# Optimization experiments

Hardware: AMD Instinct MI355X
Metric: run time of the kernel (lower is better)

## Reference

```python
import jax, jax.numpy as jnp
import numpy as np

B, T, D = 4, 2048, 2048
K, D_B, TOPK, WINDOW = 7, 128, 16, 64
GATE_CAP = 1.0
STRAND_CAP = 1.0
_PHI = 1.618033988749895
_PSI = -0.6180339887498949


def _ln(x, g, b, eps=1e-5):
    m = jnp.mean(x, axis=-1, keepdims=True)
    v = jnp.mean((x - m) ** 2, axis=-1, keepdims=True)
    return (x - m) * jax.lax.rsqrt(v + eps) * g + b


def setup_inputs() -> dict:
    ks = jax.random.split(jax.random.key(0), 20)
    rn = lambda k, s, sc=1.0: jax.random.normal(k, s, jnp.float32) * sc
    d_s = 1.0 / np.sqrt(D)
    db_s = 1.0 / np.sqrt(D_B)
    return {
        'X_write': rn(ks[0], (B, T, D)),
        'X_read': rn(ks[1], (B, T, D)),
        'slots': rn(ks[2], (B, K, D_B)),
        'W0': rn(ks[3], (D, D), d_s),
        'ln_write_g': jnp.ones((D,), jnp.float32),
        'ln_write_b': jnp.zeros((D,), jnp.float32),
        'Wv': rn(ks[4], (D_B, D), d_s),
        'Wk': rn(ks[5], (D_B, D_B), db_s),
        'slot_key_bias': rn(ks[6], (K, D_B), 2.0),
        'Wg_w': rn(ks[7], (D_B, 2 * D_B), 1.0 / np.sqrt(2 * D_B)),
        'Wg_b': jnp.full((D_B,), -2.0, jnp.float32),
        'ln_strand_g': jnp.ones((D_B,), jnp.float32),
        'ln_strand_b': jnp.zeros((D_B,), jnp.float32),
        'Wsq': rn(ks[8], (D_B, D_B), db_s),
        'Wsk': rn(ks[9], (D_B, D_B), db_s),
        'Wsv': rn(ks[10], (D_B, D_B), db_s),
        'lambda_strand': rn(ks[11], (D_B,), 0.1),
        'Wq_read': rn(ks[12], (D_B, D), d_s),
        'Wk_read': rn(ks[13], (D_B, D_B), db_s),
        'Wv_read': rn(ks[14], (D, D_B), db_s),
        'render_coeffs': rn(ks[15], (K, 3, D), 0.1),
        'slot_temps': 1.0 + rn(ks[16], (K,), 0.1),
    }


def reference(X_write, X_read, slots, W0, ln_write_g, ln_write_b, Wv, Wk,
              slot_key_bias, Wg_w, Wg_b, ln_strand_g, ln_strand_b,
              Wsq, Wsk, Wsv, lambda_strand, Wq_read, Wk_read, Wv_read,
              render_coeffs, slot_temps):
    b, t, d = X_write.shape
    sd = 1.0 / np.sqrt(D_B)
    X_n = _ln(X_write, ln_write_g, ln_write_b)

    # --- banded salience + topk (torch.no_grad region; only int indices escape) ---
    W_eff = min(WINDOW, t - 1)
    Xs = jax.lax.stop_gradient(X_n)
    X_W0 = Xs @ jax.lax.stop_gradient(W0).T            # [b,t,d]
    Xp = jnp.pad(X_W0, ((0, 0), (W_eff, 0), (0, 0)))   # left-pad so offset w -> j = i + w - W

    def band_dot(w):
        return jnp.einsum('btd,btd->bt', Xs,
                          jax.lax.dynamic_slice_in_dim(Xp, w, t, axis=1))

    band = jax.vmap(band_dot)(jnp.arange(W_eff)).transpose(1, 2, 0)  # [b,t,W]
    ii = jnp.arange(t)[:, None]
    ww = jnp.arange(W_eff)[None, :]
    jj = ii + ww - W_eff
    valid = (jj >= 0) & (ii >= 1)                      # j in [max(0,i-W), i)
    sal = jnp.where(valid, band, -jnp.inf).reshape(b, -1)
    topk_eff = min(TOPK, t * (t - 1) // 2)
    _, idx = jax.lax.top_k(sal, topk_eff)              # [b,topk]
    i_idx = idx // W_eff
    j_idx = i_idx + (idx % W_eff) - W_eff

    # --- topk pair gather + bilinear relation ---
    x_new = jnp.take_along_axis(X_n, i_idx[..., None], axis=1)  # [b,topk,d]
    x_old = jnp.take_along_axis(X_n, j_idx[..., None], axis=1)
    pair_sal = jnp.sum(x_new * (x_old @ jax.lax.stop_gradient(W0).T), axis=-1)
    alpha = jax.nn.softmax(pair_sal, axis=-1)
    R_t = jnp.einsum('bp,bpe->be', alpha, (x_new - x_old) @ Wv.T)  # [b,d_b]

    # --- slot write ---
    slot_keys = slots @ Wk.T + slot_key_bias[None]
    compat = jnp.einsum('bke,be->bk', slot_keys, R_t) * sd
    compat = compat * jax.nn.softplus(slot_temps)[None]
    sw = jax.nn.softmax(compat, axis=-1)
    weighted_R = sw[..., None] * R_t[:, None, :]                 # [b,K,d_b]
    g = jax.nn.sigmoid(jnp.concatenate([slots, weighted_R], -1) @ Wg_w.T + Wg_b)
    slots_upd = (1.0 - g) * slots + g * weighted_R

    # --- strand mixer (KxK self-attention) ---
    B_ln = _ln(slots_upd, ln_strand_g, ln_strand_b)
    att = jax.nn.softmax(jnp.einsum('bke,bme->bkm', B_ln @ Wsq.T, B_ln @ Wsk.T) * sd, axis=-1)
    ctx = att @ (B_ln @ Wsv.T)
    slots_next = slots_upd + ctx * jnp.clip(jnp.tanh(lambda_strand), -STRAND_CAP, STRAND_CAP)

    # --- aux losses ---
    L_persist = jnp.mean((slots_next - slots) ** 2)
    nrm = jnp.linalg.norm(slots_next, axis=-1, keepdims=True)
    Bn = slots_next / jnp.maximum(nrm, 1e-12)
    cos = jnp.einsum('bke,bme->bkm', Bn, Bn)
    off = 1.0 - jnp.eye(K, dtype=cos.dtype)
    L_div = jnp.sum(cos ** 2 * off) / (b * K * (K - 1))

    # --- directional render gate + read ---
    q_r = X_read @ Wq_read.T                    # [b,t,d_b]
    k_r = slots_next @ Wk_read.T                # [b,K,d_b]
    v_r = slots_next @ Wv_read.T                # [b,K,d]
    scores = jnp.einsum('bte,bke->btk', q_r, k_r) * sd
    q_mean = jnp.mean(X_read, axis=1)           # [b,d]
    w0q = q_mean @ jax.lax.stop_gradient(W0).T
    dphi = _PHI - _PSI
    phi_q = (w0q - _PSI * q_mean) / dphi
    psi_q = (_PHI * q_mean - w0q) / dphi
    pm = jnp.linalg.norm(phi_q, axis=-1, keepdims=True)
    sm = jnp.linalg.norm(psi_q, axis=-1, keepdims=True)
    tot = pm + sm + 1e-6
    basis = jnp.concatenate([jnp.ones_like(pm), pm / tot, sm / tot], axis=-1)  # [b,3]
    gate = jnp.clip(jnp.tanh(jnp.einsum('bi,kid->bkd', basis, render_coeffs)),
                    -GATE_CAP, GATE_CAP)
    z = jnp.einsum('btk,bkd->btd', jax.nn.softmax(scores, axis=-1), v_r * gate)
    return z, slots_next, L_persist, L_div
```

## Files before the change

kernel.cpp:

```cpp
#include <hip/hip_runtime.h>
#include <cstdint>
#include <cstddef>

#define DEV __device__ __forceinline__

typedef __bf16 bf16x8 __attribute__((ext_vector_type(8)));
typedef float f32x4 __attribute__((ext_vector_type(4)));
typedef unsigned short u16;
typedef unsigned int u32;

constexpr int Bq = 4, Tq = 2048, Dq = 2048, Kq = 7, DB = 128, TK = 16;
constexpr float SD = 0.08838834764831845f;
constexpr float PHIc = 1.618033988749895f;
constexpr float PSIc = -0.6180339887498949f;
constexpr float DPHI = 2.2360679774997896f;
#define NEG_INF (-__builtin_inff())

DEV u16 f2bf(float f) {
  union { float f; u32 u; } x; x.f = f;
  u32 r = (x.u + 0x7fffu + ((x.u >> 16) & 1u)) >> 16;
  return (u16)r;
}
DEV float bfbits2f(u32 h) { union { u32 u; float f; } x; x.u = h << 16; return x.f; }

DEV void async16(void* l, const void* g) {
  __builtin_amdgcn_global_load_lds((const __attribute__((address_space(1))) void*)g,
                                   (__attribute__((address_space(3))) void*)l, 16, 0, 0);
}

__global__ __launch_bounds__(256) void k_w0b(const float* __restrict__ W0, u16* __restrict__ W0b) {
  size_t i = ((size_t)blockIdx.x * 256 + threadIdx.x) * 8;
  float4 a = *(const float4*)&W0[i];
  float4 c = *(const float4*)&W0[i + 4];
  u32 p0 = (u32)f2bf(a.x) | ((u32)f2bf(a.y) << 16);
  u32 p1 = (u32)f2bf(a.z) | ((u32)f2bf(a.w) << 16);
  u32 p2 = (u32)f2bf(c.x) | ((u32)f2bf(c.y) << 16);
  u32 p3 = (u32)f2bf(c.z) | ((u32)f2bf(c.w) << 16);
  uint4 st; st.x = p0; st.y = p1; st.z = p2; st.w = p3;
  *(uint4*)&W0b[i] = st;
}

__global__ __launch_bounds__(256) void k_ln(const float* __restrict__ X, const float* __restrict__ g,
                                            const float* __restrict__ bb, u16* __restrict__ Xn) {
  int row = blockIdx.x;
  const float* xr = X + (size_t)row * Dq;
  int tid = threadIdx.x, lane = tid & 63, w = tid >> 6;
  float4 a = *(const float4*)&xr[tid * 8];
  float4 c = *(const float4*)&xr[tid * 8 + 4];
  float s = a.x + a.y + a.z + a.w + c.x + c.y + c.z + c.w;
  float q = a.x*a.x + a.y*a.y + a.z*a.z + a.w*a.w + c.x*c.x + c.y*c.y + c.z*c.z + c.w*c.w;
  #pragma unroll
  for (int o = 32; o; o >>= 1) { s += __shfl_xor(s, o); q += __shfl_xor(q, o); }
  __shared__ float red[8];
  if (lane == 0) { red[w] = s; red[w + 4] = q; }
  __syncthreads();
  float S = red[0] + red[1] + red[2] + red[3];
  float Q = red[4] + red[5] + red[6] + red[7];
  float mean = S * (1.0f / Dq);
  float var = Q * (1.0f / Dq) - mean * mean;
  float rstd = rsqrtf(var + 1e-5f);
  float v[8] = {a.x, a.y, a.z, a.w, c.x, c.y, c.z, c.w};
  u32 p[4];
  #pragma unroll
  for (int j = 0; j < 4; ++j) {
    int d0 = tid * 8 + j * 2;
    float o0 = (v[j*2]   - mean) * rstd * g[d0]   + bb[d0];
    float o1 = (v[j*2+1] - mean) * rstd * g[d0+1] + bb[d0+1];
    p[j] = (u32)f2bf(o0) | ((u32)f2bf(o1) << 16);
  }
  uint4 st; st.x = p[0]; st.y = p[1]; st.z = p[2]; st.w = p[3];
  *(uint4*)&Xn[(size_t)row * Dq + tid * 8] = st;
}

__global__ __launch_bounds__(256) void k_qmean1(const float* __restrict__ X, float* __restrict__ part) {
  int s = blockIdx.x;
  int y = blockIdx.y;
  int b = blockIdx.z;
  int tid = threadIdx.x;
  const float* xb = X + (size_t)b * Tq * Dq + (size_t)s * 1024 + tid * 4;
  f32x4 acc = {0.f, 0.f, 0.f, 0.f};
  #pragma unroll 4
  for (int t = 0; t < 64; ++t) {
    const float4 v = *(const float4*)&xb[(size_t)(y * 64 + t) * Dq];
    acc[0] += v.x; acc[1] += v.y; acc[2] += v.z; acc[3] += v.w;
  }
  float4 st; st.x = acc[0]; st.y = acc[1]; st.z = acc[2]; st.w = acc[3];
  *(float4*)&part[((size_t)(b * 32 + y)) * Dq + s * 1024 + tid * 4] = st;
}

__global__ __launch_bounds__(256) void k_qmean2(const float* __restrict__ part, float* __restrict__ qm) {
  int s = blockIdx.x, b = blockIdx.y, tid = threadIdx.x;
  int col = s * 1024 + tid * 4;
  f32x4 acc = {0.f, 0.f, 0.f, 0.f};
  #pragma unroll 8
  for (int y = 0; y < 32; ++y) {
    float4 v = *(const float4*)&part[((size_t)(b * 32 + y)) * Dq + col];
    acc[0] += v.x; acc[1] += v.y; acc[2] += v.z; acc[3] += v.w;
  }
  float4 st;
  st.x = acc[0] * (1.0f / Tq); st.y = acc[1] * (1.0f / Tq);
  st.z = acc[2] * (1.0f / Tq); st.w = acc[3] * (1.0f / Tq);
  *(float4*)&qm[(size_t)b * Dq + col] = st;
}

__global__ __launch_bounds__(256) void k_w0q(const float* __restrict__ W0, const float* __restrict__ qm,
                                             float* __restrict__ w0q) {
  __shared__ float qs[4][Dq];
  int tid = threadIdx.x, lane = tid & 63, w = tid >> 6;
  for (int i = tid * 4; i < 4 * Dq; i += 1024) {
    *(float4*)&((float*)qs)[i] = *(const float4*)&qm[i];
  }
  __syncthreads();
  #pragma unroll
  for (int r = 0; r < 8; ++r) {
    int d = blockIdx.x * 32 + w * 8 + r;
    const float* wr = W0 + (size_t)d * Dq;
    float a0 = 0, a1 = 0, a2 = 0, a3 = 0;
    for (int e = lane * 4; e < Dq; e += 256) {
      float4 wv = *(const float4*)&wr[e];
      float4 q0 = *(const float4*)&qs[0][e];
      float4 q1 = *(const float4*)&qs[1][e];
      float4 q2 = *(const float4*)&qs[2][e];
      float4 q3 = *(const float4*)&qs[3][e];
      a0 += wv.x*q0.x + wv.y*q0.y + wv.z*q0.z + wv.w*q0.w;
      a1 += wv.x*q1.x + wv.y*q1.y + wv.z*q1.z + wv.w*q1.w;
      a2 += wv.x*q2.x + wv.y*q2.y + wv.z*q2.z + wv.w*q2.w;
      a3 += wv.x*q3.x + wv.y*q3.y + wv.z*q3.z + wv.w*q3.w;
    }
    #pragma unroll
    for (int o = 32; o; o >>= 1) {
      a0 += __shfl_xor(a0, o); a1 += __shfl_xor(a1, o);
      a2 += __shfl_xor(a2, o); a3 += __shfl_xor(a3, o);
    }
    if (lane == 0) {
      w0q[0 * Dq + d] = a0; w0q[1 * Dq + d] = a1;
      w0q[2 * Dq + d] = a2; w0q[3 * Dq + d] = a3;
    }
  }
}

__global__ __launch_bounds__(256) void k_basis(const float* __restrict__ qm, const float* __restrict__ w0q,
                                               float* __restrict__ basis) {
  int tid = threadIdx.x;
  __shared__ float red[256];
  __shared__ float psum;
  for (int b = 0; b < 4; ++b) {
    float ps = 0, ss = 0;
    for (int d = tid; d < Dq; d += 256) {
      float qv = qm[b * Dq + d], wv = w0q[b * Dq + d];
      float ph = (wv - PSIc * qv) * (1.0f / DPHI);
      float pv = (PHIc * qv - wv) * (1.0f / DPHI);
      ps += ph * ph; ss += pv * pv;
    }
    red[tid] = ps; __syncthreads();
    for (int st = 128; st; st >>= 1) { if (tid < st) red[tid] += red[tid + st]; __syncthreads(); }
    if (tid == 0) psum = red[0];
    __syncthreads();
    red[tid] = ss; __syncthreads();
    for (int st = 128; st; st >>= 1) { if (tid < st) red[tid] += red[tid + st]; __syncthreads(); }
    if (tid == 0) {
      float pm = sqrtf(psum), sm = sqrtf(red[0]);
      float tot = pm + sm + 1e-6f;
      basis[b * 3 + 0] = 1.0f; basis[b * 3 + 1] = pm / tot; basis[b * 3 + 2] = sm / tot;
    }
    __syncthreads();
  }
}

__global__ __launch_bounds__(256) void k_gemm(const u16* __restrict__ A, const u16* __restrict__ B,
                                              u16* __restrict__ C, int M, int N, int K) {
  __shared__ u16 As[128 * 64], Bs[128 * 64];
  int tid = threadIdx.x, lane = tid & 63, w = tid >> 6, wr = w >> 1, wc = w & 1;
  int bm = blockIdx.x, bn = blockIdx.y;
  const u16* Ab = A + (size_t)bm * 128 * K;
  const u16* Bb = B + (size_t)bn * 128 * K;
  f32x4 zero = {0.f, 0.f, 0.f, 0.f};
  f32x4 acc[4][4];
  #pragma unroll
  for (int mi = 0; mi < 4; ++mi)
    #pragma unroll
    for (int ni = 0; ni < 4; ++ni) acc[mi][ni] = zero;
  int ro = tid >> 3;
  int co = (tid & 7) * 8;
  int cs = co ^ ((ro & 7) * 8);
  for (int k0 = 0; k0 < K; k0 += 64) {
    #pragma unroll
    for (int i = 0; i < 4; ++i) {
      int row = ro + i * 32;
      async16(&As[row * 64 + co], Ab + (size_t)row * K + k0 + cs);
      async16(&Bs[row * 64 + co], Bb + (size_t)row * K + k0 + cs);
    }
    __syncthreads();
    #pragma unroll
    for (int ks = 0; ks < 2; ++ks) {
      int cbase = ks * 32 + ((lane >> 4) * 8);
      int crd = cbase ^ ((lane & 7) * 8);
      bf16x8 af[4], bfr[4];
      #pragma unroll
      for (int mi = 0; mi < 4; ++mi)
        af[mi] = *(const bf16x8*)&As[(wr * 64 + mi * 16 + (lane & 15)) * 64 + crd];
      #pragma unroll
      for (int ni = 0; ni < 4; ++ni)
        bfr[ni] = *(const bf16x8*)&Bs[(wc * 64 + ni * 16 + (lane & 15)) * 64 + crd];
      #pragma unroll
      for (int mi = 0; mi < 4; ++mi)
        #pragma unroll
        for (int ni = 0; ni < 4; ++ni)
          acc[mi][ni] = __builtin_amdgcn_mfma_f32_16x16x32_bf16(af[mi], bfr[ni], acc[mi][ni], 0, 0, 0);
    }
    __syncthreads();
  }
  int r0 = bm * 128 + wr * 64, c0 = bn * 128 + wc * 64;
  #pragma unroll
  for (int mi = 0; mi < 4; ++mi)
    #pragma unroll
    for (int ni = 0; ni < 4; ++ni) {
      int col = c0 + ni * 16 + (lane & 15);
      int rb = r0 + mi * 16 + ((lane >> 4) * 4);
      #pragma unroll
      for (int rg = 0; rg < 4; ++rg)
        C[(size_t)(rb + rg) * N + col] = f2bf(acc[mi][ni][rg]);
    }
}

__global__ __launch_bounds__(512) void k_band(const u16* __restrict__ Xn, const u16* __restrict__ XW0,
                                              float* __restrict__ sal) {
  int b = blockIdx.y, i0 = blockIdx.x * 32;
  int tid = threadIdx.x, lane = tid & 63, w = tid >> 6;
  int mi0, ni0, mi1 = -1, ni1 = -1;
  if (w < 4)      { mi0 = 0; ni0 = w;     mi1 = 1; ni1 = w + 2; }
  else if (w < 6) { mi0 = 0; ni0 = w; }
  else            { mi0 = 1; ni0 = w - 6; }
  const u16* Xb = Xn + (size_t)b * Tq * Dq;
  const u16* Wb = XW0 + (size_t)b * Tq * Dq;
  int koff = (lane >> 4) * 8;
  const u16* ap0 = Xb + (size_t)(i0 + mi0 * 16 + (lane & 15)) * Dq + koff;
  const u16* ap1 = Xb + (size_t)(i0 + 16 + (lane & 15)) * Dq + koff;
  int j0 = i0 - 64 + ni0 * 16 + (lane & 15); j0 = min(max(j0, 0), Tq - 1);
  int j1 = i0 - 64 + (ni1 < 0 ? 0 : ni1) * 16 + (lane & 15); j1 = min(max(j1, 0), Tq - 1);
  const u16* bp0 = Wb + (size_t)j0 * Dq + koff;
  const u16* bp1 = Wb + (size_t)j1 * Dq + koff;
  f32x4 zero = {0.f, 0.f, 0.f, 0.f};
  f32x4 acc0 = zero, acc1 = zero;
  if (mi1 >= 0) {
    for (int k = 0; k < Dq; k += 32) {
      bf16x8 a0 = *(const bf16x8*)(ap0 + k);
      bf16x8 b0 = *(const bf16x8*)(bp0 + k);
      acc0 = __builtin_amdgcn_mfma_f32_16x16x32_bf16(a0, b0, acc0, 0, 0, 0);
      bf16x8 a1 = *(const bf16x8*)(ap1 + k);
      bf16x8 b1 = *(const bf16x8*)(bp1 + k);
      acc1 = __builtin_amdgcn_mfma_f32_16x16x32_bf16(a1, b1, acc1, 0, 0, 0);
    }
  } else {
    for (int k = 0; k < Dq; k += 32) {
      bf16x8 a0 = *(const bf16x8*)(ap0 + k);
      bf16x8 b0 = *(const bf16x8*)(bp0 + k);
      acc0 = __builtin_amdgcn_mfma_f32_16x16x32_bf16(a0, b0, acc0, 0, 0, 0);
    }
  }
  auto store_tile = [&](int mi, int ni, const f32x4& acc) {
    int nl = ni * 16 + (lane & 15);
    #pragma unroll
    for (int rg = 0; rg < 4; ++rg) {
      int i = i0 + mi * 16 + (lane >> 4) * 4 + rg;
      int wb = nl - (i - i0);
      if (wb >= 0 && wb < 64) {
        int j = i0 - 64 + nl;
        bool valid = (j >= 0) && (i >= 1);
        sal[((size_t)b * Tq + i) * 64 + wb] = valid ? acc[rg] : NEG_INF;
      }
    }
  };
  store_tile(mi0, ni0, acc0);
  if (mi1 >= 0) store_tile(mi1, ni1, acc1);
}

__global__ __launch_bounds__(256) void k_topk1(const float* __restrict__ sal,
                                               float* __restrict__ cv, int* __restrict__ ci) {
  int b = blockIdx.y, chunk = blockIdx.x;
  int tid = threadIdx.x, lane = tid & 63;
  const float* s = sal + (size_t)b * Tq * 64 + (size_t)chunk * 1024;
  float lv[4]; int li[4];
  #pragma unroll
  for (int i = 0; i < 4; ++i) { lv[i] = NEG_INF; li[i] = -1; }
  #pragma unroll
  for (int i = 0; i < 4; ++i) {
    int e = tid + i * 256;
    float v = s[e];
    int idx = chunk * 1024 + e;
    if (v > lv[3]) {
      lv[3] = v; li[3] = idx;
      #pragma unroll
      for (int q = 3; q > 0; --q)
        if (lv[q] > lv[q - 1]) {
          float tv = lv[q]; lv[q] = lv[q - 1]; lv[q - 1] = tv;
          int t2 = li[q]; li[q] = li[q - 1]; li[q - 1] = t2;
        }
    }
  }
  __shared__ float Sv[256][4];
  __shared__ int Si[256][4];
  __shared__ int heads[256];
  #pragma unroll
  for (int i = 0; i < 4; ++i) { Sv[tid][i] = lv[i]; Si[tid][i] = li[i]; }
  heads[tid] = 0;
  __syncthreads();
  float* ov = cv + ((size_t)b * 128 + chunk) * 16;
  int* oi = ci + ((size_t)b * 128 + chunk) * 16;
  for (int r = 0; r < 16; ++r) {
    if (tid < 64) {
      float best = NEG_INF; int bl = 0; int bidx = 0x7fffffff;
      #pragma unroll
      for (int cc = 0; cc < 4; ++cc) {
        int c = lane + cc * 64;
        int h = heads[c];
        float v = (h < 4) ? Sv[c][h] : NEG_INF;
        int ix = (h < 4) ? Si[c][h] : 0x7fffffff;
        if (v > best || (v == best && ix < bidx)) { best = v; bl = c; bidx = ix; }
      }
      #pragma unroll
      for (int o = 32; o; o >>= 1) {
        float bv = __shfl_xor(best, o); int blx = __shfl_xor(bl, o); int bix = __shfl_xor(bidx, o);
        if (bv > best || (bv == best && bix < bidx)) { best = bv; bl = blx; bidx = bix; }
      }
      if (lane == 0) {
        int h = heads[bl];
        ov[r] = best; oi[r] = (h < 4) ? Si[bl][h] : -1;
        heads[bl] = h + 1;
      }
    }
    __syncthreads();
  }
}

__global__ __launch_bounds__(256) void k_topk2(const float* __restrict__ cv, const int* __restrict__ ci,
                                               int* __restrict__ ti, int* __restrict__ tj) {
  int b = blockIdx.x, tid = threadIdx.x, lane = tid & 63;
  __shared__ float Sv[128][16];
  __shared__ int Si[128][16];
  __shared__ int heads[128];
  __shared__ int ridx[16];
  for (int i = tid; i < 128 * 16; i += 256) {
    ((float*)Sv)[i] = cv[(size_t)b * 2048 + i];
    ((int*)Si)[i] = ci[(size_t)b * 2048 + i];
  }
  if (tid < 128) heads[tid] = 0;
  __syncthreads();
  for (int r = 0; r < 16; ++r) {
    if (tid < 64) {
      float best = NEG_INF; int bl = 0; int bidx = 0x7fffffff;
      #pragma unroll
      for (int cc = 0; cc < 2; ++cc) {
        int c = lane + cc * 64;
        int h = heads[c];
        float v = (h < 16) ? Sv[c][h] : NEG_INF;
        int ix = (h < 16) ? Si[c][h] : 0x7fffffff;
        if (v > best || (v == best && ix < bidx)) { best = v; bl = c; bidx = ix; }
      }
      #pragma unroll
      for (int o = 32; o; o >>= 1) {
        float bv = __shfl_xor(best, o); int blx = __shfl_xor(bl, o); int bix = __shfl_xor(bidx, o);
        if (bv > best || (bv == best && bix < bidx)) { best = bv; bl = blx; bidx = bix; }
      }
      if (lane == 0) {
        int h = heads[bl];
        ridx[r] = Si[bl][h];
        heads[bl] = h + 1;
      }
    }
    __syncthreads();
  }
  if (tid < 16) {
    int fi = ridx[tid];
    int ii = fi >> 6;
    int jj = ii + (fi & 63) - 64;
    ti[b * TK + tid] = ii;
    tj[b * TK + tid] = jj;
  }
}

__global__ __launch_bounds__(256) void k_gatherln(const float* __restrict__ X, const float* __restrict__ g,
    const float* __restrict__ bb, const int* __restrict__ ti, const int* __restrict__ tj,
    float* __restrict__ Xnew, float* __restrict__ Xold) {
  int b = blockIdx.y, p = blockIdx.x >> 1, side = blockIdx.x & 1;
  int row = side ? tj[b * TK + p] : ti[b * TK + p];
  row = min(max(row, 0), Tq - 1);
  const float* xr = X + ((size_t)(b * Tq + row)) * Dq;
  float* dst = (side ? Xold : Xnew) + ((size_t)(b * TK + p)) * Dq;
  int tid = threadIdx.x, lane = tid & 63, w = tid >> 6;
  float4 a = *(const float4*)&xr[tid * 8];
  float4 c = *(const float4*)&xr[tid * 8 + 4];
  float s = a.x + a.y + a.z + a.w + c.x + c.y + c.z + c.w;
  float q = a.x*a.x + a.y*a.y + a.z*a.z + a.w*a.w + c.x*c.x + c.y*c.y + c.z*c.z + c.w*c.w;
  #pragma unroll
  for (int o = 32; o; o >>= 1) { s += __shfl_xor(s, o); q += __shfl_xor(q, o); }
  __shared__ float red[8];
  if (lane == 0) { red[w] = s; red[w + 4] = q; }
  __syncthreads();
  float S = red[0] + red[1] + red[2] + red[3];
  float Q = red[4] + red[5] + red[6] + red[7];
  float mean = S * (1.0f / Dq);
  float var = Q * (1.0f / Dq) - mean * mean;
  float rstd = rsqrtf(var + 1e-5f);
  float v[8] = {a.x, a.y, a.z, a.w, c.x, c.y, c.z, c.w};
  float o8[8];
  #pragma unroll
  for (int j = 0; j < 8; ++j) {
    int d = tid * 8 + j;
    o8[j] = (v[j] - mean) * rstd * g[d] + bb[d];
  }
  float4 s0; s0.x = o8[0]; s0.y = o8[1]; s0.z = o8[2]; s0.w = o8[3];
  float4 s1; s1.x = o8[4]; s1.y = o8[5]; s1.z = o8[6]; s1.w = o8[7];
  *(float4*)&dst[tid * 8] = s0;
  *(float4*)&dst[tid * 8 + 4] = s1;
}

__global__ __launch_bounds__(256) void k_pairsal(const float* __restrict__ W0, const float* __restrict__ Xnew,
                                                 const float* __restrict__ Xold, float* __restrict__ psal) {
  int d0 = blockIdx.x * 64, e0 = blockIdx.y * 64;
  int tid = threadIdx.x, P = tid & 63, dg = tid >> 6;
  f32x4 xo[16];
  #pragma unroll
  for (int i = 0; i < 16; ++i)
    xo[i] = *(const f32x4*)&Xold[(size_t)P * Dq + e0 + i * 4];
  int dbase = d0 + dg * 16;
  f32x4 xn[4];
  #pragma unroll
  for (int i = 0; i < 4; ++i)
    xn[i] = *(const f32x4*)&Xnew[(size_t)P * Dq + dbase + i * 4];
  float acc = 0.f;
  #pragma unroll
  for (int dd = 0; dd < 16; ++dd) {
    int d = __builtin_amdgcn_readfirstlane(dbase + dd);
    const float* wr = W0 + (size_t)d * Dq + e0;
    float i0 = 0.f, i1 = 0.f, i2 = 0.f, i3 = 0.f;
    #pragma unroll
    for (int i = 0; i < 16; ++i) {
      float4 wv = *(const float4*)&wr[i * 4];
      i0 += wv.x * xo[i][0]; i1 += wv.y * xo[i][1];
      i2 += wv.z * xo[i][2]; i3 += wv.w * xo[i][3];
    }
    acc += xn[dd >> 2][dd & 3] * ((i0 + i1) + (i2 + i3));
  }
  __shared__ float part[4][64];
  part[dg][P] = acc;
  __syncthreads();
  if (tid < 64)
    atomicAdd(&psal[tid], part[0][tid] + part[1][tid] + part[2][tid] + part[3][tid]);
}

__global__ __launch_bounds__(256) void k_alphart(const float* __restrict__ psal, const float* __restrict__ Xnew,
    const float* __restrict__ Xold, const float* __restrict__ Wv, float* __restrict__ Rt) {
  int bx = blockIdx.x, b = blockIdx.y;
  int tid = threadIdx.x, lane = tid & 63, w = tid >> 6;
  __shared__ float al[16], xd[Dq];
  if (tid == 0) {
    float mx = NEG_INF;
    #pragma unroll
    for (int p = 0; p < 16; ++p) mx = fmaxf(mx, psal[b * 16 + p]);
    float ee[16]; float s = 0.f;
    #pragma unroll
    for (int p = 0; p < 16; ++p) { ee[p] = expf(psal[b * 16 + p] - mx); s += ee[p]; }
    #pragma unroll
    for (int p = 0; p < 16; ++p) al[p] = ee[p] / s;
  }
  __syncthreads();
  {
    int d0 = tid * 8;
    float a8[8] = {0, 0, 0, 0, 0, 0, 0, 0};
    #pragma unroll
    for (int p = 0; p < 16; ++p) {
      const float* xn = Xnew + (size_t)(b * 16 + p) * Dq + d0;
      const float* xo = Xold + (size_t)(b * 16 + p) * Dq + d0;
      float ap = al[p];
      float4 n0 = *(const float4*)xn;
      float4 n1 = *(const float4*)(xn + 4);
      float4 o0 = *(const float4*)xo;
      float4 o1 = *(const float4*)(xo + 4);
      a8[0] += ap * (n0.x - o0.x); a8[1] += ap * (n0.y - o0.y);
      a8[2] += ap * (n0.z - o0.z); a8[3] += ap * (n0.w - o0.w);
      a8[4] += ap * (n1.x - o1.x); a8[5] += ap * (n1.y - o1.y);
      a8[6] += ap * (n1.z - o1.z); a8[7] += ap * (n1.w - o1.w);
    }
    #pragma unroll
    for (int j = 0; j < 8; ++j) xd[d0 + j] = a8[j];
  }
  __syncthreads();
  int e = bx * 4 + w;
  const float* wr = Wv + (size_t)e * Dq;
  float s = 0.f;
  #pragma unroll 8
  for (int d = lane; d < Dq; d += 64) s += wr[d] * xd[d];
  #pragma unroll
  for (int o = 32; o; o >>= 1) s += __shfl_xor(s, o);
  if (lane == 0) Rt[b * DB + e] = s;
}

__global__ __launch_bounds__(1024) void k_slots(
    const float* __restrict__ slots, const float* __restrict__ Wk, const float* __restrict__ skb,
    const float* __restrict__ Wgw, const float* __restrict__ Wgb,
    const float* __restrict__ lng, const float* __restrict__ lnb,
    const float* __restrict__ Wsq, const float* __restrict__ Wsk, const float* __restrict__ Wsv,
    const float* __restrict__ lam, const float* __restrict__ temps,
    const float* __restrict__ Rt, const float* __restrict__ Wkr,
    float* __restrict__ snOut, float* __restrict__ krOut) {
  int b = blockIdx.x, tid = threadIdx.x;
  int lane = tid & 63, w = tid >> 6;
  int sub = lane & 15, quad = lane >> 4;
  __shared__ float s_s[Kq][DB], r_s[DB], sk_s[Kq][DB], cm[8], sw[8],
                   su[Kq][DB], mv[Kq][2], bnl[Kq][DB],
                   qq[Kq][DB], kks[Kq][DB], vvs[Kq][DB],
                   att[Kq][8], sn_s[Kq][DB];
  for (int i = tid; i < Kq * DB; i += 1024) ((float*)s_s)[i] = slots[(size_t)b * Kq * DB + i];
  if (tid < DB) r_s[tid] = Rt[b * DB + tid];
  __syncthreads();
  #pragma unroll
  for (int r = 0; r < 14; ++r) {
    int idx = (w * 14 + r) * 4 + quad;
    int k = idx >> 7, e = idx & 127;
    const float* wr = Wk + e * DB;
    float a = 0.f;
    #pragma unroll
    for (int j = 0; j < 8; ++j) a += wr[sub + j * 16] * s_s[k][sub + j * 16];
    a += __shfl_xor(a, 8); a += __shfl_xor(a, 4); a += __shfl_xor(a, 2); a += __shfl_xor(a, 1);
    if (sub == 0) sk_s[k][e] = a + skb[idx];
  }
  __syncthreads();
  if (w < Kq) {
    float a = sk_s[w][lane] * r_s[lane] + sk_s[w][lane + 64] * r_s[lane + 64];
    #pragma unroll
    for (int o = 32; o; o >>= 1) a += __shfl_xor(a, o);
    if (lane == 0) {
      float t = temps[w];
      cm[w] = a * SD * log1pf(expf(t));
    }
  }
  __syncthreads();
  if (tid == 0) {
    float mx = cm[0];
    for (int k = 1; k < Kq; ++k) mx = fmaxf(mx, cm[k]);
    float ee[7]; float s = 0.f;
    for (int k = 0; k < Kq; ++k) { ee[k] = expf(cm[k] - mx); s += ee[k]; }
    for (int k = 0; k < Kq; ++k) sw[k] = ee[k] / s;
  }
  __syncthreads();
  #pragma unroll
  for (int r = 0; r < 14; ++r) {
    int idx = (w * 14 + r) * 4 + quad;
    int k = idx >> 7, e = idx & 127;
    const float* wr = Wgw + e * 256;
    float swk = sw[k];
    float a = 0.f;
    #pragma unroll
    for (int j = 0; j < 16; ++j) {
      int col = sub + j * 16;
      float x = (j < 8) ? s_s[k][col] : swk * r_s[col - 128];
      a += wr[col] * x;
    }
    a += __shfl_xor(a, 8); a += __shfl_xor(a, 4); a += __shfl_xor(a, 2); a += __shfl_xor(a, 1);
    if (sub == 0) {
      a += Wgb[e];
      float gv = 1.0f / (1.0f + expf(-a));
      float wrv = swk * r_s[e];
      su[k][e] = (1.0f - gv) * s_s[k][e] + gv * wrv;
    }
  }
  __syncthreads();
  if (w < Kq) {
    float v0 = su[w][lane], v1 = su[w][lane + 64];
    float s = v0 + v1, q = v0 * v0 + v1 * v1;
    #pragma unroll
    for (int o = 32; o; o >>= 1) { s += __shfl_xor(s, o); q += __shfl_xor(q, o); }
    if (lane == 0) {
      float m = s / DB; float va = q / DB - m * m;
      mv[w][0] = m; mv[w][1] = rsqrtf(va + 1e-5f);
    }
  }
  __syncthreads();
  for (int i = tid; i < Kq * DB; i += 1024) {
    int k = i >> 7, e = i & 127;
    bnl[k][e] = (su[k][e] - mv[k][0]) * mv[k][1] * lng[e] + lnb[e];
  }
  __syncthreads();
  #pragma unroll
  for (int r = 0; r < 14; ++r) {
    int idx = (w * 14 + r) * 4 + quad;
    int k = idx >> 7, e = idx & 127;
    const float* wr1 = Wsq + e * DB;
    const float* wr2 = Wsk + e * DB;
    const float* wr3 = Wsv + e * DB;
    float a1 = 0.f, a2 = 0.f, a3 = 0.f;
    #pragma unroll
    for (int j = 0; j < 8; ++j) {
      float x = bnl[k][sub + j * 16];
      a1 += wr1[sub + j * 16] * x;
      a2 += wr2[sub + j * 16] * x;
      a3 += wr3[sub + j * 16] * x;
    }
    #pragma unroll
    for (int o = 8; o; o >>= 1) {
      a1 += __shfl_xor(a1, o); a2 += __shfl_xor(a2, o); a3 += __shfl_xor(a3, o);
    }
    if (sub == 0) { qq[k][e] = a1; kks[k][e] = a2; vvs[k][e] = a3; }
  }
  __syncthreads();
  {
    int t4 = w * 4 + quad;
    if (t4 < 49) {
      int k = t4 / 7, m = t4 % 7;
      float a = 0.f;
      #pragma unroll
      for (int j = 0; j < 8; ++j) a += qq[k][sub + j * 16] * kks[m][sub + j * 16];
      a += __shfl_xor(a, 8); a += __shfl_xor(a, 4); a += __shfl_xor(a, 2); a += __shfl_xor(a, 1);
      if (sub == 0) att[k][m] = a * SD;
    }
  }
  __syncthreads();
  if (tid < Kq) {
    float mx = att[tid][0];
    for (int m = 1; m < Kq; ++m) mx = fmaxf(mx, att[tid][m]);
    float ee[7]; float s = 0.f;
    for (int m = 0; m < Kq; ++m) { ee[m] = expf(att[tid][m] - mx); s += ee[m]; }
    for (int m = 0; m < Kq; ++m) att[tid][m] = ee[m] / s;
  }
  __syncthreads();
  for (int i = tid; i < Kq * DB; i += 1024) {
    int k = i >> 7, e = i & 127;
    float c = 0.f;
    #pragma unroll
    for (int m = 0; m < Kq; ++m) c += att[k][m] * vvs[m][e];
    float l = tanhf(lam[e]); l = fminf(fmaxf(l, -1.0f), 1.0f);
    float v = su[k][e] + c * l;
    sn_s[k][e] = v;
    snOut[(size_t)b * Kq * DB + i] = v;
  }
  __syncthreads();
  #pragma unroll
  for (int r = 0; r < 14; ++r) {
    int idx = (w * 14 + r) * 4 + quad;
    int k = idx >> 7, e = idx & 127;
    const float* wr = Wkr + e * DB;
    float a = 0.f;
    #pragma unroll
    for (int j = 0; j < 8; ++j) a += wr[sub + j * 16] * sn_s[k][sub + j * 16];
    a += __shfl_xor(a, 8); a += __shfl_xor(a, 4); a += __shfl_xor(a, 2); a += __shfl_xor(a, 1);
    if (sub == 0) krOut[(size_t)b * Kq * DB + idx] = a;
  }
}

__global__ __launch_bounds__(256) void k_mvg(const float* __restrict__ snOut, const float* __restrict__ krOut,
    const float* __restrict__ Wqr, const float* __restrict__ Wvr, const float* __restrict__ rc,
    const float* __restrict__ basis, u16* __restrict__ Mb, u16* __restrict__ Vgb) {
  int b = blockIdx.y, tid = threadIdx.x;
  int d = blockIdx.x * 256 + tid;
  __shared__ float krs[Kq][DB], sns[Kq][DB];
  for (int i = tid; i < Kq * DB; i += 256) {
    ((float*)krs)[i] = krOut[(size_t)b * Kq * DB + i];
    ((float*)sns)[i] = snOut[(size_t)b * Kq * DB + i];
  }
  __syncthreads();
  float b0 = basis[b * 3 + 0], b1 = basis[b * 3 + 1], b2 = basis[b * 3 + 2];
  float am[7] = {0, 0, 0, 0, 0, 0, 0};
  for (int e = 0; e < DB; ++e) {
    float wq = Wqr[(size_t)e * Dq + d];
    #pragma unroll
    for (int k = 0; k < 7; ++k) am[k] += krs[k][e] * wq;
  }
  float vr[7] = {0, 0, 0, 0, 0, 0, 0};
  const float* wvrow = Wvr + (size_t)d * DB;
  for (int e = 0; e < DB; ++e) {
    float wv = wvrow[e];
    #pragma unroll
    for (int k = 0; k < 7; ++k) vr[k] += sns[k][e] * wv;
  }
  #pragma unroll
  for (int k = 0; k < 7; ++k) {
    Mb[((size_t)b * 7 + k) * Dq + d] = f2bf(am[k]);
    float gt = tanhf(b0 * rc[((size_t)k * 3 + 0) * Dq + d] +
                     b1 * rc[((size_t)k * 3 + 1) * Dq + d] +
                     b2 * rc[((size_t)k * 3 + 2) * Dq + d]);
    gt = fminf(fmaxf(gt, -1.0f), 1.0f);
    Vgb[((size_t)b * 7 + k) * Dq + d] = f2bf(vr[k] * gt);
  }
}

__global__ __launch_bounds__(256) void k_losses(const float* __restrict__ slots, const float* __restrict__ sn,
                                                float* __restrict__ out2) {
  int tid = threadIdx.x;
  __shared__ float red[256];
  __shared__ float nrm[28];
  float p = 0.f;
  for (int i = tid; i < Bq * Kq * DB; i += 256) { float d = sn[i] - slots[i]; p += d * d; }
  red[tid] = p; __syncthreads();
  for (int st = 128; st; st >>= 1) { if (tid < st) red[tid] += red[tid + st]; __syncthreads(); }
  if (tid == 0) out2[0] = red[0] / (float)(Bq * Kq * DB);
  if (tid < 28) {
    int b = tid / 7, k = tid % 7;
    float s = 0.f;
    for (int e = 0; e < DB; ++e) { float v = sn[(size_t)(b * 7 + k) * DB + e]; s += v * v; }
    nrm[tid] = fmaxf(sqrtf(s), 1e-12f);
  }
  __syncthreads();
  float dv = 0.f;
  if (tid < 168) {
    int b = tid / 42, r = tid % 42;
    int k = r / 6, m = r % 6; m += (m >= k);
    float dot = 0.f;
    for (int e = 0; e < DB; ++e)
      dot += sn[(size_t)(b * 7 + k) * DB + e] * sn[(size_t)(b * 7 + m) * DB + e];
    float c = dot / (nrm[b * 7 + k] * nrm[b * 7 + m]);
    dv = c * c;
  }
  red[tid] = dv; __syncthreads();
  for (int st = 128; st; st >>= 1) { if (tid < st) red[tid] += red[tid + st]; __syncthreads(); }
  if (tid == 0) out2[1] = red[0] / 168.0f;
}

__global__ __launch_bounds__(256) void k_z(const float* __restrict__ X, const u16* __restrict__ Mb,
                                           const u16* __restrict__ Vgb, float* __restrict__ Z) {
  int b = blockIdx.y, t0 = blockIdx.x * 16;
  int tid = threadIdx.x, lane = tid & 63, w = tid >> 6;
  __shared__ u16 Ms[7 * 2048], Vs[7 * 2048];
  for (int i = tid * 4; i < 7 * 2048; i += 1024) {
    *(uint2*)&Ms[i] = *(const uint2*)&Mb[(size_t)b * 7 * 2048 + i];
    *(uint2*)&Vs[i] = *(const uint2*)&Vgb[(size_t)b * 7 * 2048 + i];
  }
  __syncthreads();
  for (int ri = 0; ri < 4; ++ri) {
    int t = t0 + ri * 4 + w;
    const float* xr = X + ((size_t)b * Tq + t) * Dq;
    float sc[7] = {0, 0, 0, 0, 0, 0, 0};
    #pragma unroll
    for (int i = 0; i < 8; ++i) {
      int d = lane * 4 + i * 256;
      float4 x = *(const float4*)&xr[d];
      #pragma unroll
      for (int k = 0; k < 7; ++k) {
        uint2 mm = *(const uint2*)&Ms[k * 2048 + d];
        sc[k] += x.x * bfbits2f(mm.x & 0xffffu) + x.y * bfbits2f(mm.x >> 16)
               + x.z * bfbits2f(mm.y & 0xffffu) + x.w * bfbits2f(mm.y >> 16);
      }
    }
    #pragma unroll
    for (int k = 0; k < 7; ++k) {
      #pragma unroll
      for (int o = 32; o; o >>= 1) sc[k] += __shfl_xor(sc[k], o);
    }
    float mx = sc[0];
    #pragma unroll
    for (int k = 1; k < 7; ++k) mx = fmaxf(mx, sc[k]);
    float pz[7]; float s = 0.f;
    #pragma unroll
    for (int k = 0; k < 7; ++k) { pz[k] = expf((sc[k] - mx) * SD); s += pz[k]; }
    float inv = 1.0f / s;
    #pragma unroll
    for (int k = 0; k < 7; ++k) pz[k] *= inv;
    float* zr = Z + ((size_t)b * Tq + t) * Dq;
    #pragma unroll
    for (int i = 0; i < 8; ++i) {
      int d = lane * 4 + i * 256;
      float4 o4; o4.x = o4.y = o4.z = o4.w = 0.f;
      #pragma unroll
      for (int k = 0; k < 7; ++k) {
        uint2 vm = *(const uint2*)&Vs[k * 2048 + d];
        float pk = pz[k];
        o4.x += pk * bfbits2f(vm.x & 0xffffu); o4.y += pk * bfbits2f(vm.x >> 16);
        o4.z += pk * bfbits2f(vm.y & 0xffffu); o4.w += pk * bfbits2f(vm.y >> 16);
      }
      *(float4*)&zr[d] = o4;
    }
  }
}

extern "C" void kernel_launch(void* const* d_in, const int* in_sizes, int n_in,
                              void* d_out, int out_size, void* d_ws, size_t ws_size,
                              hipStream_t stream) {
  const float* Xw   = (const float*)d_in[0];
  const float* Xr   = (const float*)d_in[1];
  const float* slots= (const float*)d_in[2];
  const float* W0   = (const float*)d_in[3];
  const float* lng  = (const float*)d_in[4];
  const float* lnb  = (const float*)d_in[5];
  const float* Wv   = (const float*)d_in[6];
  const float* Wk   = (const float*)d_in[7];
  const float* skb  = (const float*)d_in[8];
  const float* Wgw  = (const float*)d_in[9];
  const float* Wgb  = (const float*)d_in[10];
  const float* lsg  = (const float*)d_in[11];
  const float* lsb  = (const float*)d_in[12];
  const float* Wsq  = (const float*)d_in[13];
  const float* Wsk  = (const float*)d_in[14];
  const float* Wsv  = (const float*)d_in[15];
  const float* lam  = (const float*)d_in[16];
  const float* Wqr  = (const float*)d_in[17];
  const float* Wkr  = (const float*)d_in[18];
  const float* Wvr  = (const float*)d_in[19];
  const float* rc   = (const float*)d_in[20];
  const float* temps= (const float*)d_in[21];

  char* wsb = (char*)d_ws;
  size_t off = 0;
  auto alloc = [&](size_t bytes) -> void* {
    void* p = wsb + off;
    off += (bytes + 255) & ~(size_t)255;
    return p;
  };
  u16*   Xn   = (u16*)  alloc((size_t)Bq * Tq * Dq * 2);
  u16*   XW0  = (u16*)  alloc((size_t)Bq * Tq * Dq * 2);
  u16*   W0b  = (u16*)  alloc((size_t)Dq * Dq * 2);
  float* sal  = (float*)alloc((size_t)Bq * Tq * 64 * 4);
  int*   ti   = (int*)  alloc(Bq * TK * 4);
  int*   tj   = (int*)  alloc(Bq * TK * 4);
  float* Xnew = (float*)alloc((size_t)Bq * TK * Dq * 4);
  float* Xold = (float*)alloc((size_t)Bq * TK * Dq * 4);
  float* psal = (float*)alloc(Bq * TK * 4);
  float* Rt   = (float*)alloc(Bq * DB * 4);
  float* qm   = (float*)alloc(Bq * Dq * 4);
  float* w0q  = (float*)alloc(Bq * Dq * 4);
  float* basis= (float*)alloc(Bq * 3 * 4);
  float* krOut= (float*)alloc(Bq * Kq * DB * 4);
  u16*   Mbf  = (u16*)  alloc((size_t)Bq * Kq * Dq * 2);
  u16*   Vgb  = (u16*)  alloc((size_t)Bq * Kq * Dq * 2);
  float* cv   = (float*)alloc((size_t)Bq * 128 * 16 * 4);
  int*   ci   = (int*)  alloc((size_t)Bq * 128 * 16 * 4);
  float* part = (float*)alloc((size_t)Bq * 32 * Dq * 4);

  float* Zout = (float*)d_out;
  float* snOut = Zout + (size_t)Bq * Tq * Dq;
  float* lossOut = snOut + Bq * Kq * DB;

  k_w0b   <<<2048, 256, 0, stream>>>(W0, W0b);
  k_ln    <<<Bq * Tq, 256, 0, stream>>>(Xw, lng, lnb, Xn);
  k_qmean1<<<dim3(2, 32, Bq), 256, 0, stream>>>(Xr, part);
  k_qmean2<<<dim3(2, Bq), 256, 0, stream>>>(part, qm);
  k_w0q   <<<64, 256, 0, stream>>>(W0, qm, w0q);
  k_basis <<<1, 256, 0, stream>>>(qm, w0q, basis);
  k_gemm  <<<dim3(64, 16), 256, 0, stream>>>(Xn, W0b, XW0, Bq * Tq, Dq, Dq);
  k_band  <<<dim3(64, Bq), 512, 0, stream>>>(Xn, XW0, sal);
  k_topk1 <<<dim3(128, Bq), 256, 0, stream>>>(sal, cv, ci);
  k_topk2 <<<Bq, 256, 0, stream>>>(cv, ci, ti, tj);
  k_gatherln<<<dim3(32, Bq), 256, 0, stream>>>(Xw, lng, lnb, ti, tj, Xnew, Xold);
  hipMemsetAsync(psal, 0, Bq * TK * 4, stream);
  k_pairsal<<<dim3(32, 32), 256, 0, stream>>>(W0, Xnew, Xold, psal);
  k_alphart<<<dim3(32, Bq), 256, 0, stream>>>(psal, Xnew, Xold, Wv, Rt);
  k_slots <<<Bq, 1024, 0, stream>>>(slots, Wk, skb, Wgw, Wgb, lsg, lsb, Wsq, Wsk, Wsv,
                                    lam, temps, Rt, Wkr, snOut, krOut);
  k_mvg   <<<dim3(8, Bq), 256, 0, stream>>>(snOut, krOut, Wqr, Wvr, rc, basis, Mbf, Vgb);
  k_losses<<<1, 256, 0, stream>>>(slots, snOut, lossOut);
  k_z     <<<dim3(128, Bq), 256, 0, stream>>>(Xr, Mbf, Vgb, Zout);
}
```

Measured before the change: 439.5 us.

## Remap GEMM workgroups across XCDs and rebalance banded salience waves

The GEMM block index is permuted so that consecutive workgroups, which the hardware deals round-robin to the 8 XCDs, land on contiguous tiles per XCD and share data in each XCD's L2. The banded salience kernel moves from 8 waves with uneven tile assignments to 12 waves with one 16x16 tile each. Each wave splits its K loop across two independent accumulators to expose more MFMA parallelism. The risks are lower occupancy from the larger 768-thread blocks and the remap assuming the block count is divisible by 8.

```diff
diff --git a/kernel.cpp b/kernel.cpp
--- a/kernel.cpp
+++ b/kernel.cpp
@@ -171,7 +171,11 @@
                                               u16* __restrict__ C, int M, int N, int K) {
   __shared__ u16 As[128 * 64], Bs[128 * 64];
   int tid = threadIdx.x, lane = tid & 63, w = tid >> 6, wr = w >> 1, wc = w & 1;
-  int bm = blockIdx.x, bn = blockIdx.y;
+  int nwg = gridDim.x * gridDim.y;
+  int flat = blockIdx.y * gridDim.x + blockIdx.x;
+  int wg = (flat & 7) * (nwg >> 3) + (flat >> 3);
+  int bm = wg % gridDim.x;
+  int bn = wg / gridDim.x;
   const u16* Ab = A + (size_t)bm * 128 * K;
   const u16* Bb = B + (size_t)bn * 128 * K;
   f32x4 zero = {0.f, 0.f, 0.f, 0.f};
@@ -223,56 +227,38 @@
     }
 }
 
-__global__ __launch_bounds__(512) void k_band(const u16* __restrict__ Xn, const u16* __restrict__ XW0,
+__global__ __launch_bounds__(768) void k_band(const u16* __restrict__ Xn, const u16* __restrict__ XW0,
                                               float* __restrict__ sal) {
   int b = blockIdx.y, i0 = blockIdx.x * 32;
   int tid = threadIdx.x, lane = tid & 63, w = tid >> 6;
-  int mi0, ni0, mi1 = -1, ni1 = -1;
-  if (w < 4)      { mi0 = 0; ni0 = w;     mi1 = 1; ni1 = w + 2; }
-  else if (w < 6) { mi0 = 0; ni0 = w; }
-  else            { mi0 = 1; ni0 = w - 6; }
+  int mi = w / 6, ni = w % 6;
   const u16* Xb = Xn + (size_t)b * Tq * Dq;
   const u16* Wb = XW0 + (size_t)b * Tq * Dq;
   int koff = (lane >> 4) * 8;
-  const u16* ap0 = Xb + (size_t)(i0 + mi0 * 16 + (lane & 15)) * Dq + koff;
-  const u16* ap1 = Xb + (size_t)(i0 + 16 + (lane & 15)) * Dq + koff;
-  int j0 = i0 - 64 + ni0 * 16 + (lane & 15); j0 = min(max(j0, 0), Tq - 1);
-  int j1 = i0 - 64 + (ni1 < 0 ? 0 : ni1) * 16 + (lane & 15); j1 = min(max(j1, 0), Tq - 1);
-  const u16* bp0 = Wb + (size_t)j0 * Dq + koff;
-  const u16* bp1 = Wb + (size_t)j1 * Dq + koff;
+  const u16* ap = Xb + (size_t)(i0 + mi * 16 + (lane & 15)) * Dq + koff;
+  int j = i0 - 64 + ni * 16 + (lane & 15); j = min(max(j, 0), Tq - 1);
+  const u16* bp = Wb + (size_t)j * Dq + koff;
   f32x4 zero = {0.f, 0.f, 0.f, 0.f};
-  f32x4 acc0 = zero, acc1 = zero;
-  if (mi1 >= 0) {
-    for (int k = 0; k < Dq; k += 32) {
-      bf16x8 a0 = *(const bf16x8*)(ap0 + k);
-      bf16x8 b0 = *(const bf16x8*)(bp0 + k);
-      acc0 = __builtin_amdgcn_mfma_f32_16x16x32_bf16(a0, b0, acc0, 0, 0, 0);
-      bf16x8 a1 = *(const bf16x8*)(ap1 + k);
-      bf16x8 b1 = *(const bf16x8*)(bp1 + k);
-      acc1 = __builtin_amdgcn_mfma_f32_16x16x32_bf16(a1, b1, acc1, 0, 0, 0);
-    }
-  } else {
-    for (int k = 0; k < Dq; k += 32) {
-      bf16x8 a0 = *(const bf16x8*)(ap0 + k);
-      bf16x8 b0 = *(const bf16x8*)(bp0 + k);
-      acc0 = __builtin_amdgcn_mfma_f32_16x16x32_bf16(a0, b0, acc0, 0, 0, 0);
-    }
-  }
-  auto store_tile = [&](int mi, int ni, const f32x4& acc) {
-    int nl = ni * 16 + (lane & 15);
-    #pragma unroll
-    for (int rg = 0; rg < 4; ++rg) {
-      int i = i0 + mi * 16 + (lane >> 4) * 4 + rg;
-      int wb = nl - (i - i0);
-      if (wb >= 0 && wb < 64) {
-        int j = i0 - 64 + nl;
-        bool valid = (j >= 0) && (i >= 1);
-        sal[((size_t)b * Tq + i) * 64 + wb] = valid ? acc[rg] : NEG_INF;
-      }
-    }
-  };
-  store_tile(mi0, ni0, acc0);
-  if (mi1 >= 0) store_tile(mi1, ni1, acc1);
+  f32x4 accA = zero, accB = zero;
+  for (int k = 0; k < Dq; k += 64) {
+    bf16x8 a0 = *(const bf16x8*)(ap + k);
+    bf16x8 b0 = *(const bf16x8*)(bp + k);
+    bf16x8 a1 = *(const bf16x8*)(ap + k + 32);
+    bf16x8 b1 = *(const bf16x8*)(bp + k + 32);
+    accA = __builtin_amdgcn_mfma_f32_16x16x32_bf16(a0, b0, accA, 0, 0, 0);
+    accB = __builtin_amdgcn_mfma_f32_16x16x32_bf16(a1, b1, accB, 0, 0, 0);
+  }
+  int nl = ni * 16 + (lane & 15);
+  #pragma unroll
+  for (int rg = 0; rg < 4; ++rg) {
+    int i = i0 + mi * 16 + (lane >> 4) * 4 + rg;
+    int wb = nl - (i - i0);
+    if (wb >= 0 && wb < 64) {
+      int jj = i0 - 64 + nl;
+      bool valid = (jj >= 0) && (i >= 1);
+      sal[((size_t)b * Tq + i) * 64 + wb] = valid ? (accA[rg] + accB[rg]) : NEG_INF;
+    }
+  }
 }
 
 __global__ __launch_bounds__(256) void k_topk1(const float* __restrict__ sal,
@@ -836,7 +822,7 @@
   k_w0q   <<<64, 256, 0, stream>>>(W0, qm, w0q);
   k_basis <<<1, 256, 0, stream>>>(qm, w0q, basis);
   k_gemm  <<<dim3(64, 16), 256, 0, stream>>>(Xn, W0b, XW0, Bq * Tq, Dq, Dq);
-  k_band  <<<dim3(64, Bq), 512, 0, stream>>>(Xn, XW0, sal);
+  k_band  <<<dim3(64, Bq), 768, 0, stream>>>(Xn, XW0, sal);
   k_topk1 <<<dim3(128, Bq), 256, 0, stream>>>(sal, cv, ci);
   k_topk2 <<<Bq, 256, 0, stream>>>(cv, ci, ti, tj);
   k_gatherln<<<dim3(32, Bq), 256, 0, stream>>>(Xw, lng, lnb, ti, tj, Xnew, Xold);
```

Result: slower. 456.2 us (+3.8%).
